# Kernel tuning notes

Measured on AMD Instinct MI355X. Metric: run time of the kernel, lower is better.

The kernel has to match this reference:

```python
import jax, jax.numpy as jnp
import numpy as np


def setup_inputs() -> dict:
    key = jax.random.key(0)
    B, D = 256, 4096
    continuous_input = jax.random.normal(key, (B, D), dtype=jnp.float32)
    return {"continuous_input": continuous_input, "timesteps": 100}


def reference(continuous_input, timesteps):
    # Temporal coding: each (batch, input) pair fires exactly one spike at a
    # time determined by sigmoid(value). With num_neurons == input_dim the
    # neuron index is just the input index, so the scalar scatter in the
    # original nested Python loops is exactly a one-hot over the time axis.
    T = timesteps
    # torch .long() truncates; sigmoid*(T-1) >= 0 so floor == trunc
    spike_times = jnp.floor(jax.nn.sigmoid(continuous_input) * (T - 1)).astype(jnp.int32)  # [B, D]
    t = jnp.arange(T, dtype=jnp.int32)  # [T]
    spikes = (t[:, None, None] == spike_times[None, :, :]).astype(jnp.float32)  # [T, B, N]
    return spikes
```

## Files before the change

### kernel.cpp

```cpp
#include <hip/hip_runtime.h>
#include <math.h>


typedef __attribute__((ext_vector_type(4))) float f32x4;

__device__ __forceinline__ float sigmoidf(float x) {
    return 1.0f / (1.0f + expf(-x));
}

__global__ __launch_bounds__(256) void spike_time_kernel(
    const float* __restrict__ x, unsigned char* __restrict__ st,
    int n, float tm1) {
    const int e = (blockIdx.x * 256 + threadIdx.x) * 4;
    if (e + 3 < n) {
        f32x4 v = *reinterpret_cast<const f32x4*>(x + e);
        uchar4 s;
        s.x = (unsigned char)(int)(sigmoidf(v.x) * tm1);
        s.y = (unsigned char)(int)(sigmoidf(v.y) * tm1);
        s.z = (unsigned char)(int)(sigmoidf(v.z) * tm1);
        s.w = (unsigned char)(int)(sigmoidf(v.w) * tm1);
        *reinterpret_cast<uchar4*>(st + e) = s;
    } else {
        for (int i = e; i < n; ++i)
            st[i] = (unsigned char)(int)(sigmoidf(x[i]) * tm1);
    }
}

__global__ __launch_bounds__(256) void write_onehot_kernel(
    const unsigned char* __restrict__ st, float* __restrict__ out, int n) {
    const int t = blockIdx.y;
    const int e = (blockIdx.x * 256 + threadIdx.x) * 4;
    if (e + 3 < n) {
        uchar4 s = *reinterpret_cast<const uchar4*>(st + e);
        f32x4 o;
        o.x = (s.x == t) ? 1.0f : 0.0f;
        o.y = (s.y == t) ? 1.0f : 0.0f;
        o.z = (s.z == t) ? 1.0f : 0.0f;
        o.w = (s.w == t) ? 1.0f : 0.0f;
        *reinterpret_cast<f32x4*>(out + (size_t)t * n + e) = o;
    } else {
        for (int i = e; i < n; ++i)
            out[(size_t)t * n + i] = (st[i] == t) ? 1.0f : 0.0f;
    }
}

__global__ __launch_bounds__(256) void fused_onehot_kernel(
    const float* __restrict__ x, float* __restrict__ out, int n, float tm1) {
    const int t = blockIdx.y;
    const int e = (blockIdx.x * 256 + threadIdx.x) * 4;
    if (e + 3 < n) {
        f32x4 v = *reinterpret_cast<const f32x4*>(x + e);
        f32x4 o;
        o.x = ((int)(sigmoidf(v.x) * tm1) == t) ? 1.0f : 0.0f;
        o.y = ((int)(sigmoidf(v.y) * tm1) == t) ? 1.0f : 0.0f;
        o.z = ((int)(sigmoidf(v.z) * tm1) == t) ? 1.0f : 0.0f;
        o.w = ((int)(sigmoidf(v.w) * tm1) == t) ? 1.0f : 0.0f;
        *reinterpret_cast<f32x4*>(out + (size_t)t * n + e) = o;
    } else {
        for (int i = e; i < n; ++i)
            out[(size_t)t * n + i] = ((int)(sigmoidf(x[i]) * tm1) == t) ? 1.0f : 0.0f;
    }
}

extern "C" void kernel_launch(void* const* d_in, const int* in_sizes, int n_in,
                              void* d_out, int out_size, void* d_ws, size_t ws_size,
                              hipStream_t stream) {
    const float* x = (const float*)d_in[0];
    float* out = (float*)d_out;
    const int n = in_sizes[0];
    const int T = out_size / n;
    const float tm1 = (float)(T - 1);

    const int n4 = (n + 3) / 4;
    const int blocks_x = (n4 + 255) / 256;

    if (ws_size >= (size_t)n) {
        unsigned char* st = (unsigned char*)d_ws;
        spike_time_kernel<<<blocks_x, 256, 0, stream>>>(x, st, n, tm1);
        dim3 grid(blocks_x, T);
        write_onehot_kernel<<<grid, 256, 0, stream>>>(st, out, n);
    } else {
        dim3 grid(blocks_x, T);
        fused_onehot_kernel<<<grid, 256, 0, stream>>>(x, out, n, tm1);
    }
}
```

Measured before the change: 401.3 us.

## Replace one-hot generation with memset plus scatter of spike ones

Instead of computing every element of the [T,B,D] one-hot tensor in a compare kernel, the output is zeroed with hipMemsetAsync and a single kernel scatters 1.0 at each element's computed spike time. This removes the per-element compare work and the intermediate spike-time buffer. It adds scattered 4-byte writes that do not coalesce, and it relies on the memset's fill bandwidth being at least as good as the kernel's vector stores.

Result: slower. 467.9 us (+16.6%).

```diff
diff --git a/kernel.cpp b/kernel.cpp
--- a/kernel.cpp
+++ b/kernel.cpp
@@ -4,61 +4,28 @@
 
 typedef __attribute__((ext_vector_type(4))) float f32x4;
 
-__device__ __forceinline__ float sigmoidf(float x) {
+__device__ __forceinline__ float sigmoidf_(float x) {
     return 1.0f / (1.0f + expf(-x));
 }
 
-__global__ __launch_bounds__(256) void spike_time_kernel(
-    const float* __restrict__ x, unsigned char* __restrict__ st,
-    int n, float tm1) {
+__global__ __launch_bounds__(256) void scatter_ones_kernel(
+    const float* __restrict__ x, float* __restrict__ out, int n, float tm1) {
     const int e = (blockIdx.x * 256 + threadIdx.x) * 4;
     if (e + 3 < n) {
-        f32x4 v = *reinterpret_cast<const f32x4*>(x + e);
-        uchar4 s;
-        s.x = (unsigned char)(int)(sigmoidf(v.x) * tm1);
-        s.y = (unsigned char)(int)(sigmoidf(v.y) * tm1);
-        s.z = (unsigned char)(int)(sigmoidf(v.z) * tm1);
-        s.w = (unsigned char)(int)(sigmoidf(v.w) * tm1);
-        *reinterpret_cast<uchar4*>(st + e) = s;
+        const f32x4 v = *reinterpret_cast<const f32x4*>(x + e);
+        const int t0 = (int)(sigmoidf_(v.x) * tm1);
+        const int t1 = (int)(sigmoidf_(v.y) * tm1);
+        const int t2 = (int)(sigmoidf_(v.z) * tm1);
+        const int t3 = (int)(sigmoidf_(v.w) * tm1);
+        out[(size_t)t0 * n + (size_t)(e    )] = 1.0f;
+        out[(size_t)t1 * n + (size_t)(e + 1)] = 1.0f;
+        out[(size_t)t2 * n + (size_t)(e + 2)] = 1.0f;
+        out[(size_t)t3 * n + (size_t)(e + 3)] = 1.0f;
     } else {
-        for (int i = e; i < n; ++i)
-            st[i] = (unsigned char)(int)(sigmoidf(x[i]) * tm1);
-    }
-}
-
-__global__ __launch_bounds__(256) void write_onehot_kernel(
-    const unsigned char* __restrict__ st, float* __restrict__ out, int n) {
-    const int t = blockIdx.y;
-    const int e = (blockIdx.x * 256 + threadIdx.x) * 4;
-    if (e + 3 < n) {
-        uchar4 s = *reinterpret_cast<const uchar4*>(st + e);
-        f32x4 o;
-        o.x = (s.x == t) ? 1.0f : 0.0f;
-        o.y = (s.y == t) ? 1.0f : 0.0f;
-        o.z = (s.z == t) ? 1.0f : 0.0f;
-        o.w = (s.w == t) ? 1.0f : 0.0f;
-        *reinterpret_cast<f32x4*>(out + (size_t)t * n + e) = o;
-    } else {
-        for (int i = e; i < n; ++i)
-            out[(size_t)t * n + i] = (st[i] == t) ? 1.0f : 0.0f;
-    }
-}
-
-__global__ __launch_bounds__(256) void fused_onehot_kernel(
-    const float* __restrict__ x, float* __restrict__ out, int n, float tm1) {
-    const int t = blockIdx.y;
-    const int e = (blockIdx.x * 256 + threadIdx.x) * 4;
-    if (e + 3 < n) {
-        f32x4 v = *reinterpret_cast<const f32x4*>(x + e);
-        f32x4 o;
-        o.x = ((int)(sigmoidf(v.x) * tm1) == t) ? 1.0f : 0.0f;
-        o.y = ((int)(sigmoidf(v.y) * tm1) == t) ? 1.0f : 0.0f;
-        o.z = ((int)(sigmoidf(v.z) * tm1) == t) ? 1.0f : 0.0f;
-        o.w = ((int)(sigmoidf(v.w) * tm1) == t) ? 1.0f : 0.0f;
-        *reinterpret_cast<f32x4*>(out + (size_t)t * n + e) = o;
-    } else {
-        for (int i = e; i < n; ++i)
-            out[(size_t)t * n + i] = ((int)(sigmoidf(x[i]) * tm1) == t) ? 1.0f : 0.0f;
+        for (int i = e; i < n; ++i) {
+            const int t = (int)(sigmoidf_(x[i]) * tm1);
+            out[(size_t)t * n + (size_t)i] = 1.0f;
+        }
     }
 }
 
@@ -68,19 +35,11 @@
     const float* x = (const float*)d_in[0];
     float* out = (float*)d_out;
     const int n = in_sizes[0];
-    const int T = out_size / n;
-    const float tm1 = (float)(T - 1);
+    const float tm1 = (float)(out_size / n - 1);
+
+    hipMemsetAsync(d_out, 0, (size_t)out_size * sizeof(float), stream);
 
     const int n4 = (n + 3) / 4;
-    const int blocks_x = (n4 + 255) / 256;
-
-    if (ws_size >= (size_t)n) {
-        unsigned char* st = (unsigned char*)d_ws;
-        spike_time_kernel<<<blocks_x, 256, 0, stream>>>(x, st, n, tm1);
-        dim3 grid(blocks_x, T);
-        write_onehot_kernel<<<grid, 256, 0, stream>>>(st, out, n);
-    } else {
-        dim3 grid(blocks_x, T);
-        fused_onehot_kernel<<<grid, 256, 0, stream>>>(x, out, n, tm1);
-    }
+    const int blocks = (n4 + 255) / 256;
+    scatter_ones_kernel<<<blocks, 256, 0, stream>>>(x, out, n, tm1);
 }
```
